# Kernel optimization log

Hardware: AMD Instinct MI355X
Metric: run time of the kernel (lower is better)

The kernel has to match this reference:

```python
import jax, jax.numpy as jnp
import numpy as np
from jax import lax


def _connected_components(fg2d):
    """4-connected component labeling of a boolean mask via min-label
    propagation with pointer-jumping compression (union-find style).
    Returns flat int32 labels; each component is labeled by its minimum
    flat pixel index; background pixels get sentinel label N."""
    H, W = fg2d.shape
    N = H * W
    sent = jnp.array([N], jnp.int32)
    idx = jnp.arange(N, dtype=jnp.int32)
    lab0 = jnp.where(fg2d.reshape(-1), idx, jnp.int32(N))
    n_compress = int(np.ceil(np.log2(max(N, 2)))) + 1

    def nb_min(lab):
        l2 = lab.reshape(H, W)
        p = jnp.pad(l2, 1, constant_values=N)  # out-of-bounds -> sentinel
        m = jnp.minimum(jnp.minimum(p[:-2, 1:-1], p[2:, 1:-1]),
                        jnp.minimum(p[1:-1, :-2], p[1:-1, 2:]))
        m = jnp.minimum(l2, m)
        return jnp.where(fg2d, m, jnp.int32(N)).reshape(-1)

    def compress(_, lab):
        ext = jnp.concatenate([lab, sent])  # index N maps to sentinel
        return jnp.minimum(lab, ext[lab])

    def body(c):
        lab, _ = c
        new = nb_min(lab)
        new = lax.fori_loop(0, n_compress, compress, new)
        return (new, jnp.any(new != lab))

    lab, _ = lax.while_loop(lambda c: c[1], body, (lab0, jnp.bool_(True)))
    return lab


def setup_inputs() -> dict:
    key = jax.random.key(0)
    x = jax.random.normal(key, (1, 1536, 2048, 2), dtype=jnp.float32)
    return {"x": x}


def reference(x):
    H, W = x.shape[1], x.shape[2]
    N = H * W
    # threshold score maps
    textmap = jnp.where(x[0, :, :, 0] > 0.4, 1.0, 0.0)
    linkmap = jnp.where(x[0, :, :, 1] > 0.4, 1.0, 0.0)
    comb = jnp.clip(textmap + linkmap, 0.0, 1.0)
    # 3x3 grayscale dilation with a ones filter == 3x3 max-pool (+1 offset);
    # foreground for labeling is the binary dilation of the combined mask
    dil = lax.reduce_window(comb, jnp.float32(0.0), lax.max, (3, 3), (1, 1), 'SAME')
    fg2d = dil > 0.0
    seg = _connected_components(fg2d)  # [N], background -> segment N
    idx = jnp.arange(N, dtype=jnp.int32)
    rows = idx // W
    cols = idx % W
    ns = N + 1
    # per-component bbox via segment reductions (fused replacement for the
    # per-label full-image mask scans in the original)
    ymin = jax.ops.segment_min(rows, seg, num_segments=ns)[:N]
    ymax = jax.ops.segment_max(rows, seg, num_segments=ns)[:N]
    xmin = jax.ops.segment_min(cols, seg, num_segments=ns)[:N]
    xmax = jax.ops.segment_max(cols, seg, num_segments=ns)[:N]
    tmax = jax.ops.segment_max(textmap.reshape(-1), seg, num_segments=ns)[:N]
    count = jax.ops.segment_sum(jnp.ones((N,), jnp.int32), seg, num_segments=ns)[:N]
    h = ymax - ymin
    w = xmax - xmin
    valid = (count > 0) & (h > 4) & (w > 4) & (tmax > 0.7)
    bboxes = jnp.where(valid[:, None], jnp.stack([ymin, xmin, h, w], axis=-1), 0)
    return bboxes, valid
```

## Files before the change

kernel.cpp:

```cpp
#include <hip/hip_runtime.h>
#include <climits>
#include <stdint.h>

typedef unsigned int u32;
typedef unsigned long long u64;

#define HH 1536
#define WW 2048
#define NPIX (HH*WW)
#define WSHIFT 11
#define WPR 64
#define MAXR 64
#define RC 4096

__global__ void k_flags(const float2* __restrict__ xv,
                        u64* __restrict__ combp64, u64* __restrict__ textp64,
                        int4* __restrict__ obb, int* __restrict__ oval) {
    int gid = blockIdx.x * 256 + threadIdx.x;
    float2 f = xv[gid];
    int tx = f.x > 0.4f;
    int cb = tx | (f.y > 0.4f);
    u64 bc = __ballot(cb);
    u64 bt = __ballot(tx);
    if ((threadIdx.x & 63) == 0) {
        combp64[gid >> 6] = bc;
        textp64[gid >> 6] = bt;
    }
    obb[gid] = make_int4(0, 0, 0, 0);
    oval[gid] = 0;
}

__global__ __launch_bounds__(256) void k_rows(const u32* __restrict__ combp,
                                              const u32* __restrict__ textp,
                                              u32* __restrict__ grun,
                                              int* __restrict__ nruns) {
    __shared__ u32 sbuf[4][MAXR];
    __shared__ u32 ebuf[4][MAXR];
    int wv = threadIdx.x >> 6, l = threadIdx.x & 63;
    int r = blockIdx.x * 4 + wv;
    int base = r * WPR + l;

    u32 c0 = combp[base];
    u32 cm = (r > 0)      ? combp[base - WPR] : 0u;
    u32 cp = (r < HH - 1) ? combp[base + WPR] : 0u;
    u32 v = c0 | cm | cp;
    u32 vl = __shfl_up(v, 1);   if (l == 0)  vl = 0;
    u32 vr = __shfl_down(v, 1); if (l == 63) vr = 0;
    u32 f = v | (v << 1) | (v >> 1) | (vl >> 31) | (vr << 31);

    u32 fl = __shfl_up(f, 1);   if (l == 0)  fl = 0;
    u32 fr = __shfl_down(f, 1); if (l == 63) fr = 0;
    u32 s = f & ~((f << 1) | (fl >> 31));
    u32 e = f & ~((f >> 1) | ((fr & 1u) << 31));

    int ns = __popc(s), ne = __popc(e);
    int is = ns, ie = ne;
    #pragma unroll
    for (int o = 1; o < 64; o <<= 1) {
        int a = __shfl_up(is, o); if (l >= o) is += a;
        int b = __shfl_up(ie, o); if (l >= o) ie += b;
    }
    int ks = is - ns, ke = ie - ne;

    u32 m = s; int k = ks;
    while (m) { int b = __ffs(m) - 1; m &= m - 1; if (k < MAXR) sbuf[wv][k] = (u32)(l * 32 + b); ++k; }
    m = e; k = ke;
    while (m) { int b = __ffs(m) - 1; m &= m - 1; if (k < MAXR) ebuf[wv][k] = (u32)(l * 32 + b); ++k; }
    int nr = __shfl(is, 63);
    nr = min(nr, MAXR);
    __syncthreads();

    u32 tmine = textp[base] & f;
    u32 txtbit = 0;
    for (int kk = 0; kk < nr; ++kk) {
        int st = (int)sbuf[wv][kk], en = (int)ebuf[wv][kk];
        int lo = max(st - l * 32, 0), hi = min(en - l * 32, 31);
        u32 mask = 0;
        if (lo <= hi)
            mask = ((hi == 31) ? 0xFFFFFFFFu : ((1u << (hi + 1)) - 1u)) & ~((1u << lo) - 1u);
        int any = __any((tmine & mask) != 0);
        if (l == kk) txtbit = (u32)(any != 0);
    }
    if (l < nr)
        grun[r * MAXR + l] = sbuf[wv][l] | (ebuf[wv][l] << 11) | (txtbit << 22);
    if (l == 0) nruns[r] = nr;
}

__device__ __forceinline__ int lfind_h(int* L, int x) {
    while (true) {
        int p = L[x];
        if (p == x) return x;
        int g = L[p];
        if (g == p) return p;
        L[x] = g;
        x = g;
    }
}

__device__ __forceinline__ void lmerge(int* L, int a, int b) {
    while (true) {
        a = lfind_h(L, a);
        b = lfind_h(L, b);
        if (a == b) return;
        if (a < b) { int s = a; a = b; b = s; }
        int old = atomicMin(&L[a], b);
        if (old == a) return;
        a = old;
    }
}

__global__ __launch_bounds__(1024) void k_solveR(
        const u32* __restrict__ grun, const int* __restrict__ nruns,
        int* __restrict__ ymin_e, int* __restrict__ xmin_e,
        int* __restrict__ ymax_e, int* __restrict__ xmax_e,
        unsigned char* __restrict__ ht,
        int4* __restrict__ obb, int* __restrict__ oval) {
    __shared__ u32 rec[RC];
    __shared__ int lab[RC];
    __shared__ unsigned short rrw[RC];
    __shared__ int pA[HH], pB[HH];
    __shared__ int sred[16][5];
    __shared__ int sFlag, sR0;
    int t = threadIdx.x;

    for (int r = t; r < HH; r += 1024) pA[r] = nruns[r];
    __syncthreads();
    int* src = pA; int* dst = pB;
    for (int o = 1; o < HH; o <<= 1) {
        for (int r = t; r < HH; r += 1024)
            dst[r] = src[r] + (r >= o ? src[r - o] : 0);
        __syncthreads();
        int* tmp = src; src = dst; dst = tmp;
    }
    int NR = min(src[HH - 1], RC);

    for (int r = t; r < HH; r += 1024) {
        int hi = src[r];
        int lo = r ? src[r - 1] : 0;
        for (int gi = lo; gi < hi; ++gi) {
            if (gi < RC) {
                rec[gi] = grun[r * MAXR + (gi - lo)];
                rrw[gi] = (unsigned short)r;
            }
        }
    }
    for (int i = t; i < NR; i += 1024) lab[i] = i;
    __syncthreads();

    for (int r = t; r < HH - 1; r += 1024) {
        int i = r ? src[r - 1] : 0;
        int iEnd = src[r];
        int j = src[r], jEnd = src[r + 1];
        while (i < iEnd && j < jEnd && i < RC && j < RC) {
            u32 ra = rec[i], rb = rec[j];
            int sa = ra & 2047, ea = (ra >> 11) & 2047;
            int sb = rb & 2047, eb = (rb >> 11) & 2047;
            if (sa <= eb && sb <= ea) lmerge(lab, i, j);
            if (ea <= eb) ++i; else ++j;
        }
    }
    __syncthreads();

    for (int pass = 0; pass < 16; ++pass) {
        if (t == 0) sFlag = 0;
        __syncthreads();
        int ch = 0;
        for (int i = t; i < NR; i += 1024) {
            int p = lab[i], g = lab[p];
            if (g != p) { lab[i] = g; ch = 1; }
        }
        if (ch) sFlag = 1;
        __syncthreads();
        if (!sFlag) break;
    }
    if (t == 0) sR0 = (NR > 0) ? lab[0] : -1;
    __syncthreads();
    int R0 = sR0;

    int m0 = INT_MIN, m1 = INT_MIN, m2 = INT_MIN, m3 = INT_MIN, tx = 0;
    for (int i = t; i < NR; i += 1024) {
        int R = lab[i];
        u32 rc = rec[i];
        int s_ = rc & 2047, e_ = (rc >> 11) & 2047, tb = (int)((rc >> 22) & 1u);
        int row = rrw[i];
        if (R == R0) {
            m0 = max(m0, 2047 - row); m1 = max(m1, row + 1);
            m2 = max(m2, 2048 - s_);  m3 = max(m3, e_ + 1);
            tx |= tb;
        } else {
            int fi = ((int)rrw[R] << WSHIFT) + (int)(rec[R] & 2047);
            atomicMax(&ymin_e[fi], 2047 - row);
            atomicMax(&ymax_e[fi], row + 1);
            atomicMax(&xmin_e[fi], 2048 - s_);
            atomicMax(&xmax_e[fi], e_ + 1);
            if (tb) ht[fi] = 1;
        }
    }
    #pragma unroll
    for (int o = 32; o > 0; o >>= 1) {
        m0 = max(m0, __shfl_xor(m0, o)); m1 = max(m1, __shfl_xor(m1, o));
        m2 = max(m2, __shfl_xor(m2, o)); m3 = max(m3, __shfl_xor(m3, o));
        tx |= __shfl_xor(tx, o);
    }
    int wv = t >> 6;
    if ((t & 63) == 0) {
        sred[wv][0] = m0; sred[wv][1] = m1; sred[wv][2] = m2;
        sred[wv][3] = m3; sred[wv][4] = tx;
    }
    __threadfence();
    __syncthreads();

    if (t == 0 && R0 >= 0) {
        for (int w2 = 1; w2 < 16; ++w2) {
            m0 = max(m0, sred[w2][0]); m1 = max(m1, sred[w2][1]);
            m2 = max(m2, sred[w2][2]); m3 = max(m3, sred[w2][3]);
            tx |= sred[w2][4];
        }
        int ym = 2047 - m0, yx = m1 - 1, xm = 2048 - m2, xx = m3 - 1;
        int h = yx - ym, w = xx - xm;
        if (h > 4 && w > 4 && tx) {
            int fi = ((int)rrw[R0] << WSHIFT) + (int)(rec[R0] & 2047);
            obb[fi] = make_int4(ym, xm, h, w);
            oval[fi] = 1;
        }
    }
    for (int i = t; i < NR; i += 1024) {
        if (lab[i] == i && i != R0) {
            int fi = ((int)rrw[i] << WSHIFT) + (int)(rec[i] & 2047);
            int ym = 2047 - ymin_e[fi], yx = ymax_e[fi] - 1;
            int xm = 2048 - xmin_e[fi], xx = xmax_e[fi] - 1;
            int h = yx - ym, w = xx - xm;
            if (h > 4 && w > 4 && ht[fi] == 1) {
                obb[fi] = make_int4(ym, xm, h, w);
                oval[fi] = 1;
            }
        }
    }
}

extern "C" void kernel_launch(void* const* d_in, const int* in_sizes, int n_in,
                              void* d_out, int out_size, void* d_ws, size_t ws_size,
                              hipStream_t stream) {
    const float* x = (const float*)d_in[0];

    int* ymin_e = (int*)d_ws;
    int* xmin_e = ymin_e + NPIX;
    int* ymax_e = xmin_e + NPIX;
    int* xmax_e = ymax_e + NPIX;
    unsigned char* ht = (unsigned char*)(xmax_e + NPIX);
    u32* combp  = (u32*)(ht + NPIX);
    u32* textp  = combp + NPIX / 32;
    u32* grun   = textp + NPIX / 32;
    int* nruns  = (int*)(grun + HH * MAXR);

    int* obb  = (int*)d_out;
    int* oval = obb + (size_t)NPIX * 4;

    k_flags<<<NPIX / 256, 256, 0, stream>>>((const float2*)x, (u64*)combp,
                                            (u64*)textp, (int4*)obb, oval);
    k_rows<<<HH / 4, 256, 0, stream>>>(combp, textp, grun, nruns);
    k_solveR<<<1, 1024, 0, stream>>>(grun, nruns, ymin_e, xmin_e, ymax_e, xmax_e,
                                     ht, (int4*)obb, oval);
}
```

Before: 121.7 us.

## Fuse row-run extraction and global solve via last-block-done atomic counter

```diff
diff --git a/kernel.cpp b/kernel.cpp
--- a/kernel.cpp
+++ b/kernel.cpp
@@ -4,6 +4,7 @@
 
 typedef unsigned int u32;
 typedef unsigned long long u64;
+typedef int v4i __attribute__((ext_vector_type(4)));
 
 #define HH 1536
 #define WW 2048
@@ -12,10 +13,12 @@
 #define WPR 64
 #define MAXR 64
 #define RC 4096
+#define NB2 96
 
 __global__ void k_flags(const float2* __restrict__ xv,
                         u64* __restrict__ combp64, u64* __restrict__ textp64,
-                        int4* __restrict__ obb, int* __restrict__ oval) {
+                        v4i* __restrict__ obb, int* __restrict__ oval,
+                        int* __restrict__ done) {
     int gid = blockIdx.x * 256 + threadIdx.x;
     float2 f = xv[gid];
     int tx = f.x > 0.4f;
@@ -26,64 +29,10 @@
         combp64[gid >> 6] = bc;
         textp64[gid >> 6] = bt;
     }
-    obb[gid] = make_int4(0, 0, 0, 0);
-    oval[gid] = 0;
-}
-
-__global__ __launch_bounds__(256) void k_rows(const u32* __restrict__ combp,
-                                              const u32* __restrict__ textp,
-                                              u32* __restrict__ grun,
-                                              int* __restrict__ nruns) {
-    __shared__ u32 sbuf[4][MAXR];
-    __shared__ u32 ebuf[4][MAXR];
-    int wv = threadIdx.x >> 6, l = threadIdx.x & 63;
-    int r = blockIdx.x * 4 + wv;
-    int base = r * WPR + l;
-
-    u32 c0 = combp[base];
-    u32 cm = (r > 0)      ? combp[base - WPR] : 0u;
-    u32 cp = (r < HH - 1) ? combp[base + WPR] : 0u;
-    u32 v = c0 | cm | cp;
-    u32 vl = __shfl_up(v, 1);   if (l == 0)  vl = 0;
-    u32 vr = __shfl_down(v, 1); if (l == 63) vr = 0;
-    u32 f = v | (v << 1) | (v >> 1) | (vl >> 31) | (vr << 31);
-
-    u32 fl = __shfl_up(f, 1);   if (l == 0)  fl = 0;
-    u32 fr = __shfl_down(f, 1); if (l == 63) fr = 0;
-    u32 s = f & ~((f << 1) | (fl >> 31));
-    u32 e = f & ~((f >> 1) | ((fr & 1u) << 31));
-
-    int ns = __popc(s), ne = __popc(e);
-    int is = ns, ie = ne;
-    #pragma unroll
-    for (int o = 1; o < 64; o <<= 1) {
-        int a = __shfl_up(is, o); if (l >= o) is += a;
-        int b = __shfl_up(ie, o); if (l >= o) ie += b;
-    }
-    int ks = is - ns, ke = ie - ne;
-
-    u32 m = s; int k = ks;
-    while (m) { int b = __ffs(m) - 1; m &= m - 1; if (k < MAXR) sbuf[wv][k] = (u32)(l * 32 + b); ++k; }
-    m = e; k = ke;
-    while (m) { int b = __ffs(m) - 1; m &= m - 1; if (k < MAXR) ebuf[wv][k] = (u32)(l * 32 + b); ++k; }
-    int nr = __shfl(is, 63);
-    nr = min(nr, MAXR);
-    __syncthreads();
-
-    u32 tmine = textp[base] & f;
-    u32 txtbit = 0;
-    for (int kk = 0; kk < nr; ++kk) {
-        int st = (int)sbuf[wv][kk], en = (int)ebuf[wv][kk];
-        int lo = max(st - l * 32, 0), hi = min(en - l * 32, 31);
-        u32 mask = 0;
-        if (lo <= hi)
-            mask = ((hi == 31) ? 0xFFFFFFFFu : ((1u << (hi + 1)) - 1u)) & ~((1u << lo) - 1u);
-        int any = __any((tmine & mask) != 0);
-        if (l == kk) txtbit = (u32)(any != 0);
-    }
-    if (l < nr)
-        grun[r * MAXR + l] = sbuf[wv][l] | (ebuf[wv][l] << 11) | (txtbit << 22);
-    if (l == 0) nruns[r] = nr;
+    v4i z = {0, 0, 0, 0};
+    __builtin_nontemporal_store(z, &obb[gid]);
+    __builtin_nontemporal_store(0, &oval[gid]);
+    if (gid == 0) *done = 0;
 }
 
 __device__ __forceinline__ int lfind_h(int* L, int x) {
@@ -109,21 +58,86 @@
     }
 }
 
-__global__ __launch_bounds__(1024) void k_solveR(
-        const u32* __restrict__ grun, const int* __restrict__ nruns,
+__global__ __launch_bounds__(1024) void k_rowsolve(
+        const u32* __restrict__ combp, const u32* __restrict__ textp,
+        u32* __restrict__ grun, int* __restrict__ nruns, int* __restrict__ done,
         int* __restrict__ ymin_e, int* __restrict__ xmin_e,
         int* __restrict__ ymax_e, int* __restrict__ xmax_e,
         unsigned char* __restrict__ ht,
-        int4* __restrict__ obb, int* __restrict__ oval) {
+        v4i* __restrict__ obb, int* __restrict__ oval) {
     __shared__ u32 rec[RC];
     __shared__ int lab[RC];
     __shared__ unsigned short rrw[RC];
     __shared__ int pA[HH], pB[HH];
     __shared__ int sred[16][5];
-    __shared__ int sFlag, sR0;
+    __shared__ int sFlag, sR0, sLast;
     int t = threadIdx.x;
-
-    for (int r = t; r < HH; r += 1024) pA[r] = nruns[r];
+    int wv = t >> 6, l = t & 63;
+
+    {
+        u32* sb = rec;
+        u32* eb = rec + 1024;
+        int r = blockIdx.x * 16 + wv;
+        int base = r * WPR + l;
+
+        u32 c0 = combp[base];
+        u32 cm = (r > 0)      ? combp[base - WPR] : 0u;
+        u32 cp = (r < HH - 1) ? combp[base + WPR] : 0u;
+        u32 v = c0 | cm | cp;
+        u32 vl = __shfl_up(v, 1);   if (l == 0)  vl = 0;
+        u32 vr = __shfl_down(v, 1); if (l == 63) vr = 0;
+        u32 f = v | (v << 1) | (v >> 1) | (vl >> 31) | (vr << 31);
+
+        u32 fl = __shfl_up(f, 1);   if (l == 0)  fl = 0;
+        u32 fr = __shfl_down(f, 1); if (l == 63) fr = 0;
+        u32 s = f & ~((f << 1) | (fl >> 31));
+        u32 e = f & ~((f >> 1) | ((fr & 1u) << 31));
+
+        int ns = __popc(s), ne = __popc(e);
+        int is = ns, ie = ne;
+        #pragma unroll
+        for (int o = 1; o < 64; o <<= 1) {
+            int a = __shfl_up(is, o); if (l >= o) is += a;
+            int b = __shfl_up(ie, o); if (l >= o) ie += b;
+        }
+        int ks = is - ns, ke = ie - ne;
+
+        u32 m = s; int k = ks;
+        while (m) { int b = __ffs(m) - 1; m &= m - 1; if (k < MAXR) sb[wv * MAXR + k] = (u32)(l * 32 + b); ++k; }
+        m = e; k = ke;
+        while (m) { int b = __ffs(m) - 1; m &= m - 1; if (k < MAXR) eb[wv * MAXR + k] = (u32)(l * 32 + b); ++k; }
+        int nr = __shfl(is, 63);
+        nr = min(nr, MAXR);
+        __syncthreads();
+
+        u32 tmine = textp[base] & f;
+        u32 txtbit = 0;
+        for (int kk = 0; kk < nr; ++kk) {
+            int st = (int)sb[wv * MAXR + kk], en = (int)eb[wv * MAXR + kk];
+            int lo = max(st - l * 32, 0), hi = min(en - l * 32, 31);
+            u32 mask = 0;
+            if (lo <= hi)
+                mask = ((hi == 31) ? 0xFFFFFFFFu : ((1u << (hi + 1)) - 1u)) & ~((1u << lo) - 1u);
+            int any = __any((tmine & mask) != 0);
+            if (l == kk) txtbit = (u32)(any != 0);
+        }
+        if (l < nr)
+            grun[r * MAXR + l] = sb[wv * MAXR + l] | (eb[wv * MAXR + l] << 11) | (txtbit << 22);
+        if (l == 0) nruns[r] = nr;
+    }
+    __syncthreads();
+
+    if (t == 0) {
+        __threadfence();
+        int old = atomicAdd(done, 1);
+        sLast = (old == NB2 - 1);
+    }
+    __syncthreads();
+    if (!sLast) return;
+    __threadfence();
+
+    for (int r = t; r < HH; r += 1024)
+        pA[r] = __hip_atomic_load(&nruns[r], __ATOMIC_RELAXED, __HIP_MEMORY_SCOPE_AGENT);
     __syncthreads();
     int* src = pA; int* dst = pB;
     for (int o = 1; o < HH; o <<= 1) {
@@ -139,7 +153,8 @@
         int lo = r ? src[r - 1] : 0;
         for (int gi = lo; gi < hi; ++gi) {
             if (gi < RC) {
-                rec[gi] = grun[r * MAXR + (gi - lo)];
+                rec[gi] = __hip_atomic_load(&grun[r * MAXR + (gi - lo)],
+                                            __ATOMIC_RELAXED, __HIP_MEMORY_SCOPE_AGENT);
                 rrw[gi] = (unsigned short)r;
             }
         }
@@ -154,9 +169,9 @@
         while (i < iEnd && j < jEnd && i < RC && j < RC) {
             u32 ra = rec[i], rb = rec[j];
             int sa = ra & 2047, ea = (ra >> 11) & 2047;
-            int sb = rb & 2047, eb = (rb >> 11) & 2047;
-            if (sa <= eb && sb <= ea) lmerge(lab, i, j);
-            if (ea <= eb) ++i; else ++j;
+            int sb2 = rb & 2047, eb2 = (rb >> 11) & 2047;
+            if (sa <= eb2 && sb2 <= ea) lmerge(lab, i, j);
+            if (ea <= eb2) ++i; else ++j;
         }
     }
     __syncthreads();
@@ -202,7 +217,6 @@
         m2 = max(m2, __shfl_xor(m2, o)); m3 = max(m3, __shfl_xor(m3, o));
         tx |= __shfl_xor(tx, o);
     }
-    int wv = t >> 6;
     if ((t & 63) == 0) {
         sred[wv][0] = m0; sred[wv][1] = m1; sred[wv][2] = m2;
         sred[wv][3] = m3; sred[wv][4] = tx;
@@ -220,7 +234,8 @@
         int h = yx - ym, w = xx - xm;
         if (h > 4 && w > 4 && tx) {
             int fi = ((int)rrw[R0] << WSHIFT) + (int)(rec[R0] & 2047);
-            obb[fi] = make_int4(ym, xm, h, w);
+            v4i bb = {ym, xm, h, w};
+            obb[fi] = bb;
             oval[fi] = 1;
         }
     }
@@ -231,7 +246,8 @@
             int xm = 2048 - xmin_e[fi], xx = xmax_e[fi] - 1;
             int h = yx - ym, w = xx - xm;
             if (h > 4 && w > 4 && ht[fi] == 1) {
-                obb[fi] = make_int4(ym, xm, h, w);
+                v4i bb = {ym, xm, h, w};
+                obb[fi] = bb;
                 oval[fi] = 1;
             }
         }
@@ -252,13 +268,14 @@
     u32* textp  = combp + NPIX / 32;
     u32* grun   = textp + NPIX / 32;
     int* nruns  = (int*)(grun + HH * MAXR);
+    int* done   = nruns + HH;
 
     int* obb  = (int*)d_out;
     int* oval = obb + (size_t)NPIX * 4;
 
     k_flags<<<NPIX / 256, 256, 0, stream>>>((const float2*)x, (u64*)combp,
-                                            (u64*)textp, (int4*)obb, oval);
-    k_rows<<<HH / 4, 256, 0, stream>>>(combp, textp, grun, nruns);
-    k_solveR<<<1, 1024, 0, stream>>>(grun, nruns, ymin_e, xmin_e, ymax_e, xmax_e,
-                                     ht, (int4*)obb, oval);
-}
+                                            (u64*)textp, (v4i*)obb, oval, done);
+    k_rowsolve<<<NB2, 1024, 0, stream>>>(combp, textp, grun, nruns, done,
+                                         ymin_e, xmin_e, ymax_e, xmax_e, ht,
+                                         (v4i*)obb, oval);
+}
```

Result: no change. 122.8 us (+0.9%).
